# Kernel optimization log

Hardware: AMD Instinct MI355X
Metric: run time of the kernel (lower is better)

## Reference

```python
import jax, jax.numpy as jnp
from jax import lax
import numpy as np

ITER = 3
ALPHA = 0.5
SMOOTH = 1.0
EPS = 1e-4


def _pool(x, op, init, window, padding):
    # x: [N, C, H, W]; window/padding apply to (H, W)
    return lax.reduce_window(x, init, op, (1, 1) + window, (1, 1, 1, 1),
                             ((0, 0), (0, 0)) + padding)


def _gelu(x):
    return jax.nn.gelu(x, approximate=False)  # matches torch F.gelu (erf)


def soft_erode(img):
    # -maxpool(-x) == minpool
    p1 = _pool(img, lax.min, jnp.inf, (3, 1), ((1, 1), (0, 0)))
    p2 = _pool(img, lax.min, jnp.inf, (1, 3), ((0, 0), (1, 1)))
    return jnp.minimum(p1, p2)


def soft_dilate(img):
    return _pool(img, lax.max, -jnp.inf, (3, 3), ((1, 1), (1, 1)))


def soft_open(img):
    return soft_dilate(soft_erode(img))


def soft_skel(img, iter_):
    skel = _gelu(img - soft_open(img))
    for _ in range(iter_):
        img = soft_erode(img)
        delta = _gelu(img - soft_open(img))
        skel = skel + _gelu(delta - skel * delta)
    return skel


def dice_loss(pred, target):
    # single-class (C==1) branch: sigmoid, then per-sample dice, mean over batch
    p = jax.nn.sigmoid(pred)
    inter = jnp.sum(p * target, axis=(1, 2, 3))          # [N]
    union = jnp.sum(p, axis=(1, 2, 3)) + jnp.sum(target, axis=(1, 2, 3)) + EPS
    gd = (2.0 * inter + EPS) / union
    return jnp.mean(1.0 - gd)  # k=0 -> 1 - gd


def setup_inputs() -> dict:
    key = jax.random.key(0)
    k1, k2 = jax.random.split(key)
    y_pred = jax.random.normal(k1, (16, 1, 1024, 1024), dtype=jnp.float32)
    y_true = jax.random.uniform(k2, (16, 1, 1024, 1024), dtype=jnp.float32)
    return {"y_pred": y_pred, "y_true": y_true}


def reference(y_pred, y_true):
    skel_pred = soft_skel(y_pred, ITER)
    skel_true = soft_skel(y_true, ITER)
    tprec = (jnp.sum(skel_pred * y_true) + SMOOTH) / (jnp.sum(skel_pred) + SMOOTH)
    tsens = (jnp.sum(skel_true * y_pred) + SMOOTH) / (jnp.sum(skel_true) + SMOOTH)
    cl_dice = 1.0 - 2.0 * (tprec * tsens) / (tprec + tsens)
    return ALPHA * cl_dice + (1.0 - ALPHA) * dice_loss(y_pred, y_true)
```

## Files before the change

### kernel.cpp

```cpp
#include <hip/hip_runtime.h>
#include <math.h>


#define HH 1024
#define WW 1024
#define NIMG 16
constexpr int IMG_ELEMS = HH * WW;
constexpr int VALID = 54;
constexpr int NSTRIP = 19;
constexpr int NBAND = 8;
constexpr int ROWS_B = 128;
constexpr int NZP = 2 * NIMG;
constexpr int WAVES = NSTRIP * NBAND * NZP;
constexpr int BLKT = 256;
constexpr int NBLK = WAVES / 4;
constexpr int PSLOTS = 128;
constexpr int DSLOTS = 16;

__device__ __forceinline__ float gelu_fast(float x) {
    float u = x * x;
    float w = x * fmaf(u, -0.10180539f, -2.3048494f);
    float e = __builtin_amdgcn_exp2f(w);
    return x * __builtin_amdgcn_rcpf(1.0f + e);
}

__device__ __forceinline__ float sigmoid_fast(float x) {
    float e = __builtin_amdgcn_exp2f(x * -1.442695041f);
    return __builtin_amdgcn_rcpf(1.0f + e);
}

template <bool RE, bool CE>
__device__ __forceinline__ void step_one(
        int u, int r,
        const float* __restrict__ X, const float* __restrict__ OT,
        size_t base, int colc, int srcLane, float cm, int rb, bool PH1,
        float (&x)[4], float (&e1)[4], float (&e2)[4], float (&e3)[4],
        float (&hm1)[4], float (&hm2)[4], float (&hm3)[4], float (&hm4)[4],
        float (&sk0)[4], float (&sk1)[4], float (&sk2)[4], float (&oth)[4],
        float (&px)[2], float (&pt)[2],
        float& a0, float& a1, float& d0, float& d1, float& d2) {
    const int I0 = (u + 3) & 3, I1 = (u + 2) & 3, I2 = (u + 1) & 3, I3 = u & 3;
    const int IA = (u + 1) & 1;

    float xv = px[IA];
    {
        int rc = min(max(r + 2, 0), HH - 1);
        px[IA] = X[base + (size_t)rc * WW + colc];
    }
    x[I0] = xv;
    float tv = pt[IA];
    {
        int rc = min(max(r, 0), HH - 1);
        pt[IA] = OT[base + (size_t)rc * WW + colc];
    }

    float c1 = x[I1];
    float v1 = fminf(x[I2], xv);
    float e1v = fminf(fminf(v1, c1),
                      fminf(__shfl_up(c1, 1, 64), __shfl_down(c1, 1, 64)));
    if (CE) e1v = __shfl(e1v, srcLane, 64);
    e1[I1] = e1v;
    hm1[I1] = fmaxf(fmaxf(__shfl_up(e1v, 1, 64), e1v), __shfl_down(e1v, 1, 64));

    float c2 = e1[I2];
    float up2 = (RE && r < 3) ? c2 : e1[I3];
    float dn2 = (RE && r > 1024) ? c2 : e1v;
    float e2v = fminf(fminf(fminf(up2, dn2), c2),
                      fminf(__shfl_up(c2, 1, 64), __shfl_down(c2, 1, 64)));
    if (CE) e2v = __shfl(e2v, srcLane, 64);
    e2[I2] = e2v;
    hm2[I2] = fmaxf(fmaxf(__shfl_up(e2v, 1, 64), e2v), __shfl_down(e2v, 1, 64));

    float c3 = e2[I3];
    float up3 = (RE && r < 4) ? c3 : e2[I0];
    float dn3 = (RE && r > 1025) ? c3 : e2v;
    float e3v = fminf(fminf(fminf(up3, dn3), c3),
                      fminf(__shfl_up(c3, 1, 64), __shfl_down(c3, 1, 64)));
    if (CE) e3v = __shfl(e3v, srcLane, 64);
    e3[I3] = e3v;
    hm3[I3] = fmaxf(fmaxf(__shfl_up(e3v, 1, 64), e3v), __shfl_down(e3v, 1, 64));

    float c4 = e3[I0];
    float up4 = (RE && r < 5) ? c4 : e3[I1];
    float dn4 = (RE && r > 1026) ? c4 : e3v;
    float e4v = fminf(fminf(fminf(up4, dn4), c4),
                      fminf(__shfl_up(c4, 1, 64), __shfl_down(c4, 1, 64)));
    if (CE) e4v = __shfl(e4v, srcLane, 64);
    hm4[I0] = fmaxf(fmaxf(__shfl_up(e4v, 1, 64), e4v), __shfl_down(e4v, 1, 64));

    float d1u = (RE && r < 3) ? hm1[I2] : hm1[I3];
    float d1d = (RE && r > 1024) ? hm1[I2] : hm1[I1];
    float dil1 = fmaxf(fmaxf(d1u, hm1[I2]), d1d);
    float p0 = x[I2];
    sk0[I2] = gelu_fast(p0 - dil1);
    oth[I2] = tv;
    if (PH1 && (unsigned)(r - 2 - rb) < (unsigned)ROWS_B) {
        float pv = sigmoid_fast(p0);
        float pvm = pv * cm;
        d0 = fmaf(pvm, tv, d0);
        d1 += pvm;
        d2 = fmaf(tv, cm, d2);
    }

    float d2u = (RE && r < 4) ? hm2[I3] : hm2[I0];
    float d2d = (RE && r > 1025) ? hm2[I3] : hm2[I2];
    float dil2 = fmaxf(fmaxf(d2u, hm2[I3]), d2d);
    float dlt1 = gelu_fast(e1[I3] - dil2);
    float s0v = sk0[I3];
    sk1[I3] = s0v + gelu_fast(fmaf(-s0v, dlt1, dlt1));

    float d3u = (RE && r < 5) ? hm3[I0] : hm3[I1];
    float d3d = (RE && r > 1026) ? hm3[I0] : hm3[I3];
    float dil3 = fmaxf(fmaxf(d3u, hm3[I0]), d3d);
    float dlt2 = gelu_fast(e2[I0] - dil3);
    float s1v = sk1[I0];
    sk2[I0] = s1v + gelu_fast(fmaf(-s1v, dlt2, dlt2));

    float d4u = (RE && r < 6) ? hm4[I1] : hm4[I2];
    float d4d = (RE && r > 1027) ? hm4[I1] : hm4[I0];
    float dil4 = fmaxf(fmaxf(d4u, hm4[I1]), d4d);
    float dlt3 = gelu_fast(e3[I1] - dil4);
    float s2v = sk2[I1];
    float sfin = s2v + gelu_fast(fmaf(-s2v, dlt3, dlt3));
    if ((unsigned)(r - 5 - rb) < (unsigned)ROWS_B) {
        float sm = sfin * cm;
        a0 += sm;
        a1 = fmaf(sm, oth[I1], a1);
    }
}

template <bool CE>
__device__ __forceinline__ void run_band(
        const float* __restrict__ X, const float* __restrict__ OT,
        size_t base, int colc, int srcLane, float cm, int rb, bool PH1,
        float& a0, float& a1, float& d0, float& d1, float& d2) {
    float x[4] = {0, 0, 0, 0}, e1[4] = {0, 0, 0, 0};
    float e2[4] = {0, 0, 0, 0}, e3[4] = {0, 0, 0, 0};
    float hm1[4] = {0, 0, 0, 0}, hm2[4] = {0, 0, 0, 0};
    float hm3[4] = {0, 0, 0, 0}, hm4[4] = {0, 0, 0, 0};
    float sk0[4] = {0, 0, 0, 0}, sk1[4] = {0, 0, 0, 0};
    float sk2[4] = {0, 0, 0, 0}, oth[4] = {0, 0, 0, 0};
    float px[2], pt[2];

    const int r0 = rb - 5;
    {
        int rc = min(max(r0, 0), HH - 1);
        px[r0 & 1] = X[base + (size_t)rc * WW + colc];
        rc = min(max(r0 + 1, 0), HH - 1);
        px[(r0 + 1) & 1] = X[base + (size_t)rc * WW + colc];
        rc = min(max(r0 - 2, 0), HH - 1);
        pt[r0 & 1] = OT[base + (size_t)rc * WW + colc];
        rc = min(max(r0 - 1, 0), HH - 1);
        pt[(r0 + 1) & 1] = OT[base + (size_t)rc * WW + colc];
    }

    for (int g = 0; g < 35; g++) {
        const int rg = r0 + g * 4;
        if (rg < 6 || rg > 1021) {
#pragma unroll
            for (int u = 0; u < 4; u++)
                step_one<true, CE>(u, rg + u, X, OT, base, colc, srcLane, cm,
                                   rb, PH1, x, e1, e2, e3, hm1, hm2, hm3, hm4,
                                   sk0, sk1, sk2, oth, px, pt, a0, a1, d0, d1, d2);
        } else {
#pragma unroll
            for (int u = 0; u < 4; u++)
                step_one<false, CE>(u, rg + u, X, OT, base, colc, srcLane, cm,
                                    rb, PH1, x, e1, e2, e3, hm1, hm2, hm3, hm4,
                                    sk0, sk1, sk2, oth, px, pt, a0, a1, d0, d1, d2);
        }
    }
}

__global__ __launch_bounds__(BLKT, 4) void cl_stream(
        const float* __restrict__ y_pred,
        const float* __restrict__ y_true,
        float* __restrict__ accP,
        float* __restrict__ accD) {
    const int wv = blockIdx.x * 4 + (threadIdx.x >> 6);
    const int lane = threadIdx.x & 63;
    int tmp = wv;
    const int strip = tmp % NSTRIP; tmp /= NSTRIP;
    const int band = tmp % NBAND;   tmp /= NBAND;
    const int img = tmp & (NIMG - 1);
    const bool PH1 = tmp < NIMG;
    const float* __restrict__ X  = PH1 ? y_pred : y_true;
    const float* __restrict__ OT = PH1 ? y_true : y_pred;
    const size_t base = (size_t)img * IMG_ELEMS;

    const int col = strip * VALID - 5 + lane;
    const int colc = min(max(col, 0), WW - 1);
    const float cm = (lane >= 5 && lane <= 58 && col < WW) ? 1.0f : 0.0f;
    const int rb = band * ROWS_B;

    const int loL = max(0, 5 - strip * VALID);
    const int hiL = min(63, (WW - 1) - (strip * VALID - 5));
    const int srcLane = min(max(lane, loL), hiL);
    const bool colEdge = (loL > 0) || (hiL < 63);

    float a0 = 0.f, a1 = 0.f, d0 = 0.f, d1 = 0.f, d2 = 0.f;
    if (colEdge)
        run_band<true >(X, OT, base, colc, srcLane, cm, rb, PH1, a0, a1, d0, d1, d2);
    else
        run_band<false>(X, OT, base, colc, srcLane, cm, rb, PH1, a0, a1, d0, d1, d2);

    for (int o = 1; o < 64; o <<= 1) {
        a0 += __shfl_xor(a0, o, 64);
        a1 += __shfl_xor(a1, o, 64);
    }
    if (PH1) {
        for (int o = 1; o < 64; o <<= 1) {
            d0 += __shfl_xor(d0, o, 64);
            d1 += __shfl_xor(d1, o, 64);
            d2 += __shfl_xor(d2, o, 64);
        }
    }
    if (lane == 0) {
        int slot = (wv * 37) & (PSLOTS - 1);
        atomicAdd(&accP[slot * 32 + (PH1 ? 0 : 2)], a0);
        atomicAdd(&accP[slot * 32 + (PH1 ? 1 : 3)], a1);
        if (PH1) {
            int ds = (strip + band * 7) & (DSLOTS - 1);
            float* dst = accD + (size_t)(img * DSLOTS + ds) * 32;
            atomicAdd(&dst[0], d0);
            atomicAdd(&dst[1], d1);
            atomicAdd(&dst[2], d2);
        }
    }
}

__global__ __launch_bounds__(256) void final_combine(
        const float* __restrict__ accP,
        const float* __restrict__ accD,
        float* __restrict__ out) {
    __shared__ float shp[2][4];
    __shared__ float shd[NIMG][3];
    int tid = threadIdx.x;
    int lane = tid & 63, wave = tid >> 6;

    float p0 = 0.f, p1 = 0.f, p2 = 0.f, p3 = 0.f;
    if (tid < PSLOTS) {
        const float* s = accP + tid * 32;
        p0 = s[0]; p1 = s[1]; p2 = s[2]; p3 = s[3];
    }
    for (int o = 32; o > 0; o >>= 1) {
        p0 += __shfl_down(p0, o, 64); p1 += __shfl_down(p1, o, 64);
        p2 += __shfl_down(p2, o, 64); p3 += __shfl_down(p3, o, 64);
    }
    if (lane == 0 && wave < 2) {
        shp[wave][0] = p0; shp[wave][1] = p1; shp[wave][2] = p2; shp[wave][3] = p3;
    }

    int n = tid >> 4, s16 = tid & 15;
    const float* d = accD + (size_t)(n * DSLOTS + s16) * 32;
    float q0 = d[0], q1 = d[1], q2 = d[2];
    for (int o = 8; o > 0; o >>= 1) {
        q0 += __shfl_down(q0, o, 16);
        q1 += __shfl_down(q1, o, 16);
        q2 += __shfl_down(q2, o, 16);
    }
    if (s16 == 0) { shd[n][0] = q0; shd[n][1] = q1; shd[n][2] = q2; }
    __syncthreads();

    if (tid == 0) {
        float sumP  = shp[0][0] + shp[1][0];
        float sumPt = shp[0][1] + shp[1][1];
        float sumT  = shp[0][2] + shp[1][2];
        float sumTp = shp[0][3] + shp[1][3];
        const float SMOOTH = 1.0f;
        float tprec = (sumPt + SMOOTH) / (sumP + SMOOTH);
        float tsens = (sumTp + SMOOTH) / (sumT + SMOOTH);
        float cl = 1.0f - 2.0f * (tprec * tsens) / (tprec + tsens);
        const float EPS = 1e-4f;
        float dsum = 0.f;
        for (int k = 0; k < NIMG; k++) {
            float gd = (2.0f * shd[k][0] + EPS) / (shd[k][1] + shd[k][2] + EPS);
            dsum += 1.0f - gd;
        }
        out[0] = 0.5f * cl + 0.5f * (dsum / (float)NIMG);
    }
}

extern "C" void kernel_launch(void* const* d_in, const int* in_sizes, int n_in,
                              void* d_out, int out_size, void* d_ws, size_t ws_size,
                              hipStream_t stream) {
    const float* y_pred = (const float*)d_in[0];
    const float* y_true = (const float*)d_in[1];
    float* out = (float*)d_out;

    float* accP = (float*)d_ws;
    float* accD = accP + PSLOTS * 32;

    hipMemsetAsync(accP, 0, (PSLOTS * 32 + NIMG * DSLOTS * 32) * sizeof(float),
                   stream);

    cl_stream<<<NBLK, BLKT, 0, stream>>>(y_pred, y_true, accP, accD);
    final_combine<<<1, 256, 0, stream>>>(accP, accD, out);
}
```

Before: 261.6 us.

## Process two columns per lane with float2 loads and separable dilation

Each lane now handles two adjacent columns using float2 loads, which widens strips from 54 to 116 valid columns and cuts halo redundancy. Band geometry changes to 12 bands of 86 rows. The 3x3 dilation is made separable: a vertical max first, then one horizontal shuffle. This removes the per-level hm buffers and some shuffles per pixel. The trade-off is higher register pressure from the float2 state arrays and more complex column-edge handling through paired shuffles.

```diff
diff --git a/kernel.cpp b/kernel.cpp
--- a/kernel.cpp
+++ b/kernel.cpp
@@ -6,14 +6,15 @@
 #define WW 1024
 #define NIMG 16
 constexpr int IMG_ELEMS = HH * WW;
-constexpr int VALID = 54;
-constexpr int NSTRIP = 19;
-constexpr int NBAND = 8;
-constexpr int ROWS_B = 128;
+constexpr int VALID = 116;
+constexpr int NSTRIP = 9;
+constexpr int NBAND = 12;
+constexpr int ROWS_B = 86;
 constexpr int NZP = 2 * NIMG;
 constexpr int WAVES = NSTRIP * NBAND * NZP;
 constexpr int BLKT = 256;
 constexpr int NBLK = WAVES / 4;
+constexpr int NGROUP = 24;
 constexpr int PSLOTS = 128;
 constexpr int DSLOTS = 16;
 
@@ -29,145 +30,208 @@
     return __builtin_amdgcn_rcpf(1.0f + e);
 }
 
+__device__ __forceinline__ float2 ce_fix(float2 e, int sl0, int sl1,
+                                         bool pr0, bool pr1) {
+    float a0 = __shfl(e.x, sl0, 64), b0 = __shfl(e.y, sl0, 64);
+    float a1 = __shfl(e.x, sl1, 64), b1 = __shfl(e.y, sl1, 64);
+    float2 r;
+    r.x = pr0 ? b0 : a0;
+    r.y = pr1 ? b1 : a1;
+    return r;
+}
+
 template <bool RE, bool CE>
 __device__ __forceinline__ void step_one(
         int u, int r,
         const float* __restrict__ X, const float* __restrict__ OT,
-        size_t base, int colc, int srcLane, float cm, int rb, bool PH1,
-        float (&x)[4], float (&e1)[4], float (&e2)[4], float (&e3)[4],
-        float (&hm1)[4], float (&hm2)[4], float (&hm3)[4], float (&hm4)[4],
-        float (&sk0)[4], float (&sk1)[4], float (&sk2)[4], float (&oth)[4],
-        float (&px)[2], float (&pt)[2],
+        size_t base, int colc0, int colc1,
+        int sl0, int sl1, bool pr0, bool pr1,
+        float cmx, float cmy, int rb, int rows, bool PH1,
+        float2 (&x)[4], float2 (&e1)[4], float2 (&e2)[4], float2 (&e3)[4],
+        float2 (&e4)[4],
+        float2 (&sk0)[4], float2 (&sk1)[4], float2 (&sk2)[4], float2 (&oth)[4],
+        float2 (&px2)[2], float2 (&pt2)[2],
         float& a0, float& a1, float& d0, float& d1, float& d2) {
     const int I0 = (u + 3) & 3, I1 = (u + 2) & 3, I2 = (u + 1) & 3, I3 = u & 3;
     const int IA = (u + 1) & 1;
 
-    float xv = px[IA];
+    float2 xv = px2[IA];
     {
         int rc = min(max(r + 2, 0), HH - 1);
-        px[IA] = X[base + (size_t)rc * WW + colc];
+        size_t ro = base + (size_t)rc * WW;
+        if (CE) { px2[IA].x = X[ro + colc0]; px2[IA].y = X[ro + colc1]; }
+        else px2[IA] = *(const float2*)&X[ro + colc0];
     }
     x[I0] = xv;
-    float tv = pt[IA];
+    float2 tv = pt2[IA];
     {
         int rc = min(max(r, 0), HH - 1);
-        pt[IA] = OT[base + (size_t)rc * WW + colc];
-    }
-
-    float c1 = x[I1];
-    float v1 = fminf(x[I2], xv);
-    float e1v = fminf(fminf(v1, c1),
-                      fminf(__shfl_up(c1, 1, 64), __shfl_down(c1, 1, 64)));
-    if (CE) e1v = __shfl(e1v, srcLane, 64);
+        size_t ro = base + (size_t)rc * WW;
+        if (CE) { pt2[IA].x = OT[ro + colc0]; pt2[IA].y = OT[ro + colc1]; }
+        else pt2[IA] = *(const float2*)&OT[ro + colc0];
+    }
+
+    float2 cc = x[I1];
+    float lf = __shfl_up(cc.y, 1, 64), rt = __shfl_down(cc.x, 1, 64);
+    float2 e1v;
+    e1v.x = fminf(fminf(fminf(x[I2].x, xv.x), cc.x), fminf(lf, cc.y));
+    e1v.y = fminf(fminf(fminf(x[I2].y, xv.y), cc.y), fminf(cc.x, rt));
+    if (CE) e1v = ce_fix(e1v, sl0, sl1, pr0, pr1);
     e1[I1] = e1v;
-    hm1[I1] = fmaxf(fmaxf(__shfl_up(e1v, 1, 64), e1v), __shfl_down(e1v, 1, 64));
-
-    float c2 = e1[I2];
-    float up2 = (RE && r < 3) ? c2 : e1[I3];
-    float dn2 = (RE && r > 1024) ? c2 : e1v;
-    float e2v = fminf(fminf(fminf(up2, dn2), c2),
-                      fminf(__shfl_up(c2, 1, 64), __shfl_down(c2, 1, 64)));
-    if (CE) e2v = __shfl(e2v, srcLane, 64);
+
+    cc = e1[I2];
+    float2 up = (RE && r < 3) ? cc : e1[I3];
+    float2 dn = (RE && r > 1024) ? cc : e1v;
+    lf = __shfl_up(cc.y, 1, 64); rt = __shfl_down(cc.x, 1, 64);
+    float2 e2v;
+    e2v.x = fminf(fminf(fminf(up.x, dn.x), cc.x), fminf(lf, cc.y));
+    e2v.y = fminf(fminf(fminf(up.y, dn.y), cc.y), fminf(cc.x, rt));
+    if (CE) e2v = ce_fix(e2v, sl0, sl1, pr0, pr1);
     e2[I2] = e2v;
-    hm2[I2] = fmaxf(fmaxf(__shfl_up(e2v, 1, 64), e2v), __shfl_down(e2v, 1, 64));
-
-    float c3 = e2[I3];
-    float up3 = (RE && r < 4) ? c3 : e2[I0];
-    float dn3 = (RE && r > 1025) ? c3 : e2v;
-    float e3v = fminf(fminf(fminf(up3, dn3), c3),
-                      fminf(__shfl_up(c3, 1, 64), __shfl_down(c3, 1, 64)));
-    if (CE) e3v = __shfl(e3v, srcLane, 64);
+
+    cc = e2[I3];
+    up = (RE && r < 4) ? cc : e2[I0];
+    dn = (RE && r > 1025) ? cc : e2v;
+    lf = __shfl_up(cc.y, 1, 64); rt = __shfl_down(cc.x, 1, 64);
+    float2 e3v;
+    e3v.x = fminf(fminf(fminf(up.x, dn.x), cc.x), fminf(lf, cc.y));
+    e3v.y = fminf(fminf(fminf(up.y, dn.y), cc.y), fminf(cc.x, rt));
+    if (CE) e3v = ce_fix(e3v, sl0, sl1, pr0, pr1);
     e3[I3] = e3v;
-    hm3[I3] = fmaxf(fmaxf(__shfl_up(e3v, 1, 64), e3v), __shfl_down(e3v, 1, 64));
-
-    float c4 = e3[I0];
-    float up4 = (RE && r < 5) ? c4 : e3[I1];
-    float dn4 = (RE && r > 1026) ? c4 : e3v;
-    float e4v = fminf(fminf(fminf(up4, dn4), c4),
-                      fminf(__shfl_up(c4, 1, 64), __shfl_down(c4, 1, 64)));
-    if (CE) e4v = __shfl(e4v, srcLane, 64);
-    hm4[I0] = fmaxf(fmaxf(__shfl_up(e4v, 1, 64), e4v), __shfl_down(e4v, 1, 64));
-
-    float d1u = (RE && r < 3) ? hm1[I2] : hm1[I3];
-    float d1d = (RE && r > 1024) ? hm1[I2] : hm1[I1];
-    float dil1 = fmaxf(fmaxf(d1u, hm1[I2]), d1d);
-    float p0 = x[I2];
-    sk0[I2] = gelu_fast(p0 - dil1);
-    oth[I2] = tv;
-    if (PH1 && (unsigned)(r - 2 - rb) < (unsigned)ROWS_B) {
-        float pv = sigmoid_fast(p0);
-        float pvm = pv * cm;
-        d0 = fmaf(pvm, tv, d0);
-        d1 += pvm;
-        d2 = fmaf(tv, cm, d2);
-    }
-
-    float d2u = (RE && r < 4) ? hm2[I3] : hm2[I0];
-    float d2d = (RE && r > 1025) ? hm2[I3] : hm2[I2];
-    float dil2 = fmaxf(fmaxf(d2u, hm2[I3]), d2d);
-    float dlt1 = gelu_fast(e1[I3] - dil2);
-    float s0v = sk0[I3];
-    sk1[I3] = s0v + gelu_fast(fmaf(-s0v, dlt1, dlt1));
-
-    float d3u = (RE && r < 5) ? hm3[I0] : hm3[I1];
-    float d3d = (RE && r > 1026) ? hm3[I0] : hm3[I3];
-    float dil3 = fmaxf(fmaxf(d3u, hm3[I0]), d3d);
-    float dlt2 = gelu_fast(e2[I0] - dil3);
-    float s1v = sk1[I0];
-    sk2[I0] = s1v + gelu_fast(fmaf(-s1v, dlt2, dlt2));
-
-    float d4u = (RE && r < 6) ? hm4[I1] : hm4[I2];
-    float d4d = (RE && r > 1027) ? hm4[I1] : hm4[I0];
-    float dil4 = fmaxf(fmaxf(d4u, hm4[I1]), d4d);
-    float dlt3 = gelu_fast(e3[I1] - dil4);
-    float s2v = sk2[I1];
-    float sfin = s2v + gelu_fast(fmaf(-s2v, dlt3, dlt3));
-    if ((unsigned)(r - 5 - rb) < (unsigned)ROWS_B) {
-        float sm = sfin * cm;
-        a0 += sm;
-        a1 = fmaf(sm, oth[I1], a1);
+
+    cc = e3[I0];
+    up = (RE && r < 5) ? cc : e3[I1];
+    dn = (RE && r > 1026) ? cc : e3v;
+    lf = __shfl_up(cc.y, 1, 64); rt = __shfl_down(cc.x, 1, 64);
+    float2 e4v;
+    e4v.x = fminf(fminf(fminf(up.x, dn.x), cc.x), fminf(lf, cc.y));
+    e4v.y = fminf(fminf(fminf(up.y, dn.y), cc.y), fminf(cc.x, rt));
+    if (CE) e4v = ce_fix(e4v, sl0, sl1, pr0, pr1);
+    e4[I0] = e4v;
+
+    {
+        float2 ctr = e1[I2];
+        float2 wu = (RE && r < 3) ? ctr : e1[I3];
+        float2 wd = (RE && r > 1024) ? ctr : e1v;
+        float2 vm;
+        vm.x = fmaxf(fmaxf(wu.x, ctr.x), wd.x);
+        vm.y = fmaxf(fmaxf(wu.y, ctr.y), wd.y);
+        float lv = __shfl_up(vm.y, 1, 64), rv = __shfl_down(vm.x, 1, 64);
+        float2 p0 = x[I2];
+        float2 s;
+        s.x = gelu_fast(p0.x - fmaxf(fmaxf(lv, vm.x), vm.y));
+        s.y = gelu_fast(p0.y - fmaxf(fmaxf(vm.x, vm.y), rv));
+        sk0[I2] = s;
+        oth[I2] = tv;
+        if (PH1 && (unsigned)(r - 2 - rb) < (unsigned)rows) {
+            float pvx = sigmoid_fast(p0.x) * cmx;
+            float pvy = sigmoid_fast(p0.y) * cmy;
+            d0 = fmaf(pvx, tv.x, fmaf(pvy, tv.y, d0));
+            d1 += pvx + pvy;
+            d2 = fmaf(tv.x, cmx, fmaf(tv.y, cmy, d2));
+        }
+    }
+
+    {
+        float2 ctr = e2[I3];
+        float2 wu = (RE && r < 4) ? ctr : e2[I0];
+        float2 wd = (RE && r > 1025) ? ctr : e2v;
+        float2 vm;
+        vm.x = fmaxf(fmaxf(wu.x, ctr.x), wd.x);
+        vm.y = fmaxf(fmaxf(wu.y, ctr.y), wd.y);
+        float lv = __shfl_up(vm.y, 1, 64), rv = __shfl_down(vm.x, 1, 64);
+        float2 dlt;
+        dlt.x = gelu_fast(e1[I3].x - fmaxf(fmaxf(lv, vm.x), vm.y));
+        dlt.y = gelu_fast(e1[I3].y - fmaxf(fmaxf(vm.x, vm.y), rv));
+        float2 s0v = sk0[I3];
+        sk1[I3].x = s0v.x + gelu_fast(fmaf(-s0v.x, dlt.x, dlt.x));
+        sk1[I3].y = s0v.y + gelu_fast(fmaf(-s0v.y, dlt.y, dlt.y));
+    }
+
+    {
+        float2 ctr = e3[I0];
+        float2 wu = (RE && r < 5) ? ctr : e3[I1];
+        float2 wd = (RE && r > 1026) ? ctr : e3v;
+        float2 vm;
+        vm.x = fmaxf(fmaxf(wu.x, ctr.x), wd.x);
+        vm.y = fmaxf(fmaxf(wu.y, ctr.y), wd.y);
+        float lv = __shfl_up(vm.y, 1, 64), rv = __shfl_down(vm.x, 1, 64);
+        float2 dlt;
+        dlt.x = gelu_fast(e2[I0].x - fmaxf(fmaxf(lv, vm.x), vm.y));
+        dlt.y = gelu_fast(e2[I0].y - fmaxf(fmaxf(vm.x, vm.y), rv));
+        float2 s1v = sk1[I0];
+        sk2[I0].x = s1v.x + gelu_fast(fmaf(-s1v.x, dlt.x, dlt.x));
+        sk2[I0].y = s1v.y + gelu_fast(fmaf(-s1v.y, dlt.y, dlt.y));
+    }
+
+    {
+        float2 ctr = e4[I1];
+        float2 wu = (RE && r < 6) ? ctr : e4[I2];
+        float2 wd = (RE && r > 1027) ? ctr : e4v;
+        float2 vm;
+        vm.x = fmaxf(fmaxf(wu.x, ctr.x), wd.x);
+        vm.y = fmaxf(fmaxf(wu.y, ctr.y), wd.y);
+        float lv = __shfl_up(vm.y, 1, 64), rv = __shfl_down(vm.x, 1, 64);
+        float2 dlt;
+        dlt.x = gelu_fast(e3[I1].x - fmaxf(fmaxf(lv, vm.x), vm.y));
+        dlt.y = gelu_fast(e3[I1].y - fmaxf(fmaxf(vm.x, vm.y), rv));
+        float2 s2v = sk2[I1];
+        float sx = s2v.x + gelu_fast(fmaf(-s2v.x, dlt.x, dlt.x));
+        float sy = s2v.y + gelu_fast(fmaf(-s2v.y, dlt.y, dlt.y));
+        if ((unsigned)(r - 5 - rb) < (unsigned)rows) {
+            float mx = sx * cmx, my = sy * cmy;
+            float2 o5 = oth[I1];
+            a0 += mx + my;
+            a1 = fmaf(mx, o5.x, fmaf(my, o5.y, a1));
+        }
     }
 }
 
 template <bool CE>
 __device__ __forceinline__ void run_band(
         const float* __restrict__ X, const float* __restrict__ OT,
-        size_t base, int colc, int srcLane, float cm, int rb, bool PH1,
+        size_t base, int colc0, int colc1, int sl0, int sl1, bool pr0, bool pr1,
+        float cmx, float cmy, int rb, int rows, bool PH1,
         float& a0, float& a1, float& d0, float& d1, float& d2) {
-    float x[4] = {0, 0, 0, 0}, e1[4] = {0, 0, 0, 0};
-    float e2[4] = {0, 0, 0, 0}, e3[4] = {0, 0, 0, 0};
-    float hm1[4] = {0, 0, 0, 0}, hm2[4] = {0, 0, 0, 0};
-    float hm3[4] = {0, 0, 0, 0}, hm4[4] = {0, 0, 0, 0};
-    float sk0[4] = {0, 0, 0, 0}, sk1[4] = {0, 0, 0, 0};
-    float sk2[4] = {0, 0, 0, 0}, oth[4] = {0, 0, 0, 0};
-    float px[2], pt[2];
+    float2 z; z.x = 0.f; z.y = 0.f;
+    float2 x[4] = {z, z, z, z}, e1[4] = {z, z, z, z}, e2[4] = {z, z, z, z},
+           e3[4] = {z, z, z, z}, e4[4] = {z, z, z, z},
+           sk0[4] = {z, z, z, z}, sk1[4] = {z, z, z, z}, sk2[4] = {z, z, z, z},
+           oth[4] = {z, z, z, z};
+    float2 px2[2], pt2[2];
 
     const int r0 = rb - 5;
     {
-        int rc = min(max(r0, 0), HH - 1);
-        px[r0 & 1] = X[base + (size_t)rc * WW + colc];
-        rc = min(max(r0 + 1, 0), HH - 1);
-        px[(r0 + 1) & 1] = X[base + (size_t)rc * WW + colc];
-        rc = min(max(r0 - 2, 0), HH - 1);
-        pt[r0 & 1] = OT[base + (size_t)rc * WW + colc];
-        rc = min(max(r0 - 1, 0), HH - 1);
-        pt[(r0 + 1) & 1] = OT[base + (size_t)rc * WW + colc];
-    }
-
-    for (int g = 0; g < 35; g++) {
+        auto ld = [&](const float* __restrict__ P, int rr) -> float2 {
+            int rc = min(max(rr, 0), HH - 1);
+            size_t ro = base + (size_t)rc * WW;
+            float2 v;
+            if (CE) { v.x = P[ro + colc0]; v.y = P[ro + colc1]; }
+            else v = *(const float2*)&P[ro + colc0];
+            return v;
+        };
+        px2[r0 & 1] = ld(X, r0);
+        px2[(r0 + 1) & 1] = ld(X, r0 + 1);
+        pt2[r0 & 1] = ld(OT, r0 - 2);
+        pt2[(r0 + 1) & 1] = ld(OT, r0 - 1);
+    }
+
+    for (int g = 0; g < NGROUP; g++) {
         const int rg = r0 + g * 4;
         if (rg < 6 || rg > 1021) {
 #pragma unroll
             for (int u = 0; u < 4; u++)
-                step_one<true, CE>(u, rg + u, X, OT, base, colc, srcLane, cm,
-                                   rb, PH1, x, e1, e2, e3, hm1, hm2, hm3, hm4,
-                                   sk0, sk1, sk2, oth, px, pt, a0, a1, d0, d1, d2);
+                step_one<true, CE>(u, rg + u, X, OT, base, colc0, colc1,
+                                   sl0, sl1, pr0, pr1, cmx, cmy, rb, rows, PH1,
+                                   x, e1, e2, e3, e4, sk0, sk1, sk2, oth,
+                                   px2, pt2, a0, a1, d0, d1, d2);
         } else {
 #pragma unroll
             for (int u = 0; u < 4; u++)
-                step_one<false, CE>(u, rg + u, X, OT, base, colc, srcLane, cm,
-                                    rb, PH1, x, e1, e2, e3, hm1, hm2, hm3, hm4,
-                                    sk0, sk1, sk2, oth, px, pt, a0, a1, d0, d1, d2);
+                step_one<false, CE>(u, rg + u, X, OT, base, colc0, colc1,
+                                    sl0, sl1, pr0, pr1, cmx, cmy, rb, rows, PH1,
+                                    x, e1, e2, e3, e4, sk0, sk1, sk2, oth,
+                                    px2, pt2, a0, a1, d0, d1, d2);
         }
     }
 }
@@ -188,21 +252,25 @@
     const float* __restrict__ OT = PH1 ? y_true : y_pred;
     const size_t base = (size_t)img * IMG_ELEMS;
 
-    const int col = strip * VALID - 5 + lane;
-    const int colc = min(max(col, 0), WW - 1);
-    const float cm = (lane >= 5 && lane <= 58 && col < WW) ? 1.0f : 0.0f;
+    const int sbase = strip * VALID - 6;
+    const int c0 = sbase + 2 * lane, c1 = c0 + 1;
+    const int cc0 = min(max(c0, 0), WW - 1), cc1 = min(max(c1, 0), WW - 1);
+    const int dd0 = cc0 - sbase, dd1 = cc1 - sbase;
+    const int sl0 = dd0 >> 1, sl1 = dd1 >> 1;
+    const bool pr0 = (dd0 & 1) != 0, pr1 = (dd1 & 1) != 0;
+    const bool colEdge = (strip == 0) || (strip == NSTRIP - 1);
+    const float cmx = (lane >= 3 && lane <= 60 && c0 < WW) ? 1.0f : 0.0f;
+    const float cmy = (lane >= 3 && lane <= 60 && c1 < WW) ? 1.0f : 0.0f;
     const int rb = band * ROWS_B;
-
-    const int loL = max(0, 5 - strip * VALID);
-    const int hiL = min(63, (WW - 1) - (strip * VALID - 5));
-    const int srcLane = min(max(lane, loL), hiL);
-    const bool colEdge = (loL > 0) || (hiL < 63);
+    const int rows = min(ROWS_B, HH - rb);
 
     float a0 = 0.f, a1 = 0.f, d0 = 0.f, d1 = 0.f, d2 = 0.f;
     if (colEdge)
-        run_band<true >(X, OT, base, colc, srcLane, cm, rb, PH1, a0, a1, d0, d1, d2);
+        run_band<true >(X, OT, base, cc0, cc1, sl0, sl1, pr0, pr1,
+                        cmx, cmy, rb, rows, PH1, a0, a1, d0, d1, d2);
     else
-        run_band<false>(X, OT, base, colc, srcLane, cm, rb, PH1, a0, a1, d0, d1, d2);
+        run_band<false>(X, OT, base, cc0, cc1, sl0, sl1, pr0, pr1,
+                        cmx, cmy, rb, rows, PH1, a0, a1, d0, d1, d2);
 
     for (int o = 1; o < 64; o <<= 1) {
         a0 += __shfl_xor(a0, o, 64);
```

Result: slower. 280.5 us (+7.2%).
